# Kernel optimization log

Hardware: AMD Instinct MI355X
Metric: run time of the kernel (lower is better)

## Reference

```python
import jax, jax.numpy as jnp
import numpy as np

B, L, D, H, E, M, P = 2, 512, 768, 12, 32, 4, 256
EMB, BS, MAP, C = 768, 64, 256, 97


def setup_inputs() -> dict:
    key = jax.random.key(0)
    ks = jax.random.split(key, 16)
    w = lambda k, s: (0.02 * jax.random.normal(k, s, jnp.float32))
    seq = jax.random.normal(ks[0], (B, L, D), jnp.float32)
    attn = jax.random.uniform(ks[1], (B, H, L, L), jnp.float32)
    entity_pos = jax.random.randint(ks[2], (B, E, M), 0, L - 2)
    # distinct (h, t) entity pairs per document -> unique mention-pair scatter slots
    grid = jnp.stack(jnp.meshgrid(jnp.arange(E), jnp.arange(E), indexing='ij'), -1).reshape(-1, 2)
    hts = jnp.stack([grid[jax.random.permutation(jax.random.fold_in(ks[3], b), E * E)[:P]] for b in range(B)], 0)
    mention_idx = jnp.broadcast_to(jnp.arange(E * M).reshape(E, M), (B, E, M))
    return {
        'seq': seq, 'attn': attn,
        'entity_pos': entity_pos, 'hts': hts, 'mention_idx': mention_idx,
        'W_head': w(ks[4], (2 * D, EMB)), 'b_head': jnp.zeros((EMB,), jnp.float32),
        'W_tail': w(ks[5], (2 * D, EMB)), 'b_tail': jnp.zeros((EMB,), jnp.float32),
        'W_rel': w(ks[6], (EMB * BS, C)), 'b_rel': jnp.zeros((C,), jnp.float32),
        'W_fh': w(ks[7], (D, EMB)), 'W_ft': w(ks[8], (D, EMB)), 'b_f': jnp.zeros((EMB,), jnp.float32),
        'W_unet': w(ks[9], (EMB, C)), 'b_unet': jnp.zeros((C,), jnp.float32),
        'W_mlp': w(ks[10], (EMB, C)), 'b_mlp': jnp.zeros((C,), jnp.float32),
        'W_bil': w(ks[11], (3 * C, C)), 'b_bil': jnp.zeros((C,), jnp.float32),
    }


def reference(seq, attn, entity_pos, hts, mention_idx,
              W_head, b_head, W_tail, b_tail, W_rel, b_rel,
              W_fh, W_ft, b_f, W_unet, b_unet, W_mlp, b_mlp, W_bil, b_bil):
    pos = entity_pos + 1                                 # bert offset
    b3 = jnp.arange(B)[:, None, None]
    ment_emb = seq[b3, pos]                              # [B,E,M,D] mention gather
    ment_att = attn[b3, :, pos]                          # [B,E,M,H,L]
    ent_emb = jax.nn.logsumexp(ment_emb, axis=2)         # [B,E,D] logsumexp pool
    ent_att = ment_att.mean(axis=2)                      # [B,E,H,L]
    b2 = jnp.arange(B)[:, None]
    h_idx, t_idx = hts[..., 0], hts[..., 1]
    hs, ts = ent_emb[b2, h_idx], ent_emb[b2, t_idx]      # [B,P,D]
    ha, ta = ent_att[b2, h_idx], ent_att[b2, t_idx]      # [B,P,H,L]
    ht_att = (ha * ta).mean(2)                           # [B,P,L]
    ht_att = ht_att / (ht_att.sum(-1, keepdims=True) + 1e-5)
    rs = jnp.einsum('bld,bpl->bpd', seq, ht_att)         # localized context
    N = B * P
    hz = jnp.tanh(jnp.concatenate([hs, rs], -1).reshape(N, 2 * D) @ W_head + b_head)
    tz = jnp.tanh(jnp.concatenate([ts, rs], -1).reshape(N, 2 * D) @ W_tail + b_tail)
    bl = (hz.reshape(N, EMB // BS, BS, 1) * tz.reshape(N, EMB // BS, 1, BS)).reshape(N, EMB * BS)
    r1 = bl @ W_rel + b_rel                              # [N,C]
    # mention-pair dense map scatter (map_rss)
    ment_flat = ment_emb.reshape(B, E * M, D)
    mh = mention_idx[b2, h_idx]                          # [B,P,M]
    mt = mention_idx[b2, t_idx]
    mh2 = jnp.broadcast_to(mh[:, :, :, None], (B, P, M, M))
    mt2 = jnp.broadcast_to(mt[:, :, None, :], (B, P, M, M))
    b4 = jnp.broadcast_to(jnp.arange(B)[:, None, None, None], (B, P, M, M))
    eh = ment_flat[b4, mh2]                              # [B,P,M,M,D]
    et = ment_flat[b4, mt2]
    feat = eh @ W_fh + et @ W_ft + b_f                   # fused Linear(cat(h,t))
    mp = jnp.zeros((B, MAP, MAP, EMB), seq.dtype).at[b4, mh2, mt2].set(feat)
    enc2 = jnp.tanh(mp @ W_unet + b_unet)                # UNet-channel surrogate
    enc3 = jax.nn.gelu(mp @ W_mlp + b_mlp)               # MLP-channel surrogate
    r2 = jax.nn.logsumexp(enc2[b4, mh2, mt2], axis=(2, 3)).reshape(N, C)
    r3 = jax.nn.logsumexp(enc3[b4, mh2, mt2], axis=(2, 3)).reshape(N, C)
    return jnp.concatenate([r1, r2, r3], -1) @ W_bil + b_bil
```

## Files before the change

kernel.cpp:

```cpp
#include <hip/hip_runtime.h>
#include <hip/hip_bf16.h>

#define B_  2
#define L_  512
#define D_  768
#define H_  12
#define E_  32
#define M_  4
#define P_  256
#define EMB_ 768
#define BS_ 64
#define C_  97
#define N_  (B_*P_)

#define KTOT_    49152
#define CPAD_    112
#define KSPLIT_  48
#define KCHUNK_  (KTOT_/KSPLIT_)
#define PSTR_    128
#define TILE_    (CPAD_*64)

typedef __hip_bfloat16 bf16;
typedef __attribute__((ext_vector_type(8))) short bf16x8;
typedef __attribute__((ext_vector_type(4))) float f32x4;
typedef __attribute__((ext_vector_type(8))) float f32x8;

__device__ inline float ldIn(const void* p, long idx, int isbf) {
    return isbf ? (float)((const bf16*)p)[idx] : ((const float*)p)[idx];
}

__device__ inline unsigned short f2bf(float f) {
    bf16 h = (bf16)f;
    return *(unsigned short*)&h;
}

__device__ inline void cvt16(unsigned short* o, float4 a, float4 b, float4 c, float4 d) {
    o[0]=f2bf(a.x);  o[1]=f2bf(a.y);  o[2]=f2bf(a.z);  o[3]=f2bf(a.w);
    o[4]=f2bf(b.x);  o[5]=f2bf(b.y);  o[6]=f2bf(b.z);  o[7]=f2bf(b.w);
    o[8]=f2bf(c.x);  o[9]=f2bf(c.y);  o[10]=f2bf(c.z); o[11]=f2bf(c.w);
    o[12]=f2bf(d.x); o[13]=f2bf(d.y); o[14]=f2bf(d.z); o[15]=f2bf(d.w);
}

__device__ inline int detect_bf(const void* seqd) {
    const unsigned short* u = (const unsigned short*)seqd;
    int lane = threadIdx.x & 63;
    unsigned short e = (u[lane] >> 7) & 0xFF;
    unsigned long long m = __ballot(e >= 140);
    return m == 0ull;
}

struct PrepArgs {
    const void* src[8];
    long off[8];
    int K[8];
    int Ncols[8];
    int Npad[8];
    unsigned short* dst[8];
    const void* W_bil;  float* W_bilF;
    const void* b_f; const void* W_unet; const void* b_unet;
    const void* W_mlp; const void* b_mlp; float* c23p;
    const void* W_rel; unsigned short* WBt;
    const void* seqd;
    const void* attn; const int* entity_pos; const int* hts;
    unsigned short* mentb; float* ent_emb; unsigned short* htb;
};

union PrepSm {
    float T[32][65];
    unsigned short TW[CPAD_][80];
    float red[256];
};

__global__ void prep_kernel(PrepArgs a) {
    int isbf = detect_bf(a.seqd);
    int z = blockIdx.z;
    __shared__ PrepSm sm;
    int tid = threadIdx.x;
    if (z == 0) {
        int lin = blockIdx.y*48 + blockIdx.x;
        if (lin >= 16) return;
        int c = tid;
        if (c >= C_) return;
        float s2 = 0.f, s3 = 0.f;
        int d0 = lin*48;
        for (int i = 0; i < 48; i++) {
            int d = d0 + i;
            float bf = ldIn(a.b_f, d, isbf);
            s2 += bf * ldIn(a.W_unet, (long)d*C_ + c, isbf);
            s3 += bf * ldIn(a.W_mlp,  (long)d*C_ + c, isbf);
        }
        if (lin == 0) {
            s2 += ldIn(a.b_unet, c, isbf);
            s3 += ldIn(a.b_mlp,  c, isbf);
        }
        a.c23p[lin*194 + c]      = s2;
        a.c23p[lin*194 + 97 + c] = s3;
    } else if (z == 1) {
        int lin = blockIdx.y*48 + blockIdx.x;
        if (lin >= KTOT_/64) return;
        int k0 = lin * 64;
        for (int idx = tid; idx < 64*97; idx += 256) {
            int kk = idx / 97, c = idx % 97;
            sm.TW[c][kk] = f2bf(ldIn(a.W_rel, (long)(k0+kk)*C_ + c, isbf));
        }
        for (int idx = tid; idx < 15*64; idx += 256) {
            sm.TW[97 + (idx>>6)][idx & 63] = 0;
        }
        __syncthreads();
        unsigned short* tb = a.WBt + (long)lin*TILE_;
        for (int t = 0; t < 4; t++) {
            int idx = tid + t*256;
            if (idx < 896) {
                int l  = idx & 63;
                int h  = (idx >> 6) & 1;
                int ct = idx >> 7;
                int row = ct*16 + (l & 15);
                int col = h*32 + (l >> 4)*8;
                *(uint4*)(tb + idx*8) = *(uint4*)&sm.TW[row][col];
            }
        }
    } else if (z <= 9) {
        int j = z - 2;
        int K = a.K[j], Ncols = a.Ncols[j], Npad = a.Npad[j];
        int k0 = blockIdx.x*32, n0 = blockIdx.y*64;
        if (k0 >= K || n0 >= Npad) return;
        const void* src = a.src[j];
        long off = a.off[j];
        unsigned short* dst = a.dst[j];
        int r = tid >> 3, c8 = (tid & 7) * 8;
        if ((Ncols & 7) == 0) {
            long base = off + (long)(k0+r)*Ncols + n0 + c8;
            if (isbf) {
                unsigned short tmp[8];
                *(uint4*)tmp = *(const uint4*)((const unsigned short*)src + base);
                #pragma unroll
                for (int e = 0; e < 8; e++) {
                    bf16 hh = *(bf16*)&tmp[e];
                    sm.T[r][c8+e] = (float)hh;
                }
            } else {
                const float* sp = (const float*)src + base;
                float4 x = *(const float4*)sp;
                float4 y = *(const float4*)(sp + 4);
                sm.T[r][c8+0]=x.x; sm.T[r][c8+1]=x.y; sm.T[r][c8+2]=x.z; sm.T[r][c8+3]=x.w;
                sm.T[r][c8+4]=y.x; sm.T[r][c8+5]=y.y; sm.T[r][c8+6]=y.z; sm.T[r][c8+7]=y.w;
            }
        } else {
            #pragma unroll
            for (int e = 0; e < 8; e++) {
                int n = n0 + c8 + e;
                sm.T[r][c8+e] = (n < Ncols) ? ldIn(src, off + (long)(k0+r)*Ncols + n, isbf) : 0.f;
            }
        }
        __syncthreads();
        int nn = tid >> 2, q8 = (tid & 3) * 8;
        unsigned short o[8];
        #pragma unroll
        for (int e = 0; e < 8; e++) o[e] = f2bf(sm.T[q8+e][nn]);
        *(uint4*)(dst + (long)(n0+nn)*K + k0 + q8) = *(uint4*)o;
    } else if (z == 10) {
        int lin = blockIdx.y*48 + blockIdx.x;
        int idx = lin*256 + tid;
        if (idx < 291*C_) a.W_bilF[idx] = ldIn(a.W_bil, idx, isbf);
    } else {
        int lin = blockIdx.y*48 + blockIdx.x;
        if (lin >= 576) return;
        if (lin < 512) {
            int bp = lin;
            int b = bp >> 8;
            int h_e = a.hts[bp*2+0], t_e = a.hts[bp*2+1];
            int ph[M_], pt[M_];
            for (int m = 0; m < M_; m++) {
                ph[m] = a.entity_pos[(b*E_ + h_e)*M_ + m] + 1;
                pt[m] = a.entity_pos[(b*E_ + t_e)*M_ + m] + 1;
            }
            float v[2];
            for (int t = 0; t < 2; t++) {
                int l = tid + t*256;
                float s = 0.f;
                for (int h = 0; h < H_; h++) {
                    long hb = ((long)(b*H_ + h))*L_;
                    float ha = 0.f, ta = 0.f;
                    for (int m = 0; m < M_; m++) {
                        ha += ldIn(a.attn, (hb + ph[m])*L_ + l, isbf);
                        ta += ldIn(a.attn, (hb + pt[m])*L_ + l, isbf);
                    }
                    s += ha * ta;
                }
                v[t] = s * (0.0625f / H_);
            }
            sm.red[tid] = v[0] + v[1];
            __syncthreads();
            for (int off = 128; off > 0; off >>= 1) {
                if (tid < off) sm.red[tid] += sm.red[tid+off];
                __syncthreads();
            }
            float inv = 1.0f / (sm.red[0] + 1e-5f);
            for (int t = 0; t < 2; t++) {
                int l = tid + t*256;
                a.htb[(long)bp*L_ + l] = f2bf(v[t] * inv);
            }
        } else {
            int be = lin - 512;
            int b = be >> 5;
            int pos[M_];
            for (int m = 0; m < M_; m++) pos[m] = a.entity_pos[be*M_+m] + 1;
            for (int d = tid; d < D_; d += 256) {
                float x[M_];
                for (int m = 0; m < M_; m++) {
                    x[m] = ldIn(a.seqd, ((long)b*L_ + pos[m])*D_ + d, isbf);
                    a.mentb[((long)be*M_ + m)*D_ + d] = f2bf(x[m]);
                }
                float mx = fmaxf(fmaxf(x[0],x[1]), fmaxf(x[2],x[3]));
                float s = expf(x[0]-mx)+expf(x[1]-mx)+expf(x[2]-mx)+expf(x[3]-mx);
                a.ent_emb[(long)be*D_ + d] = mx + logf(s);
            }
        }
    }
}

struct MfmaJob {
    const unsigned short* A[8];
    const unsigned short* Bt[8];
    const void* bias[8];
    void* C[8];
    const void* seqd;
    const int* hts;
    const float* ent_emb;
    const float* rsrc;
    int K[8];
    int ldc[8];
    int act[8];
    int obf[8];
    int Mt[8];
    int Nt[8];
    int gath[8];
};

__global__ void mfma_nt2_kernel(MfmaJob args) {
    int z = blockIdx.z;
    int m0 = blockIdx.x*32, n0 = blockIdx.y*32;
    if (m0 >= args.Mt[z] || n0 >= args.Nt[z]) return;
    int isbf = detect_bf(args.seqd);
    const unsigned short* A  = args.A[z];
    const unsigned short* Bt = args.Bt[z];
    const void* bias = args.bias[z];
    void* C = args.C[z];
    int K = args.K[z], ldc = args.ldc[z], act = args.act[z], obf = args.obf[z];
    int gmode = args.gath[z];
    __shared__ unsigned short Al[2][32][136];
    __shared__ unsigned short Btl[2][32][136];
    int tid = threadIdx.x, wave = tid>>6, lane = tid&63;
    int lm = lane&15, lq = lane>>4;
    int rowg = wave>>1, cgrp = wave&1;
    int rr = tid >> 3;
    int kc = (tid & 7) * 16;
    const float *gh = nullptr, *gr = nullptr;
    if (gmode) {
        int m = m0 + rr, b = m >> 8;
        int ent = args.hts[m*2 + (gmode-1)];
        gh = args.ent_emb + (long)(b*E_ + ent)*D_ + kc;
        gr = args.rsrc + (long)m*EMB_ + kc;
    }
    uint4 ra0, ra1, rb0, rb1;
    float4 fa0, fa1, fa2, fa3;

    if (gmode) {
        fa0 = *(const float4*)gh;      fa1 = *(const float4*)(gh+4);
        fa2 = *(const float4*)(gh+8);  fa3 = *(const float4*)(gh+12);
        unsigned short o[16];
        cvt16(o, fa0, fa1, fa2, fa3);
        *(uint4*)&Al[0][rr][kc]   = *(uint4*)o;
        *(uint4*)&Al[0][rr][kc+8] = *(uint4*)(o+8);
    } else {
        ra0 = *(const uint4*)(A + (long)(m0+rr)*K + kc);
        ra1 = *(const uint4*)(A + (long)(m0+rr)*K + kc + 8);
        *(uint4*)&Al[0][rr][kc]   = ra0;
        *(uint4*)&Al[0][rr][kc+8] = ra1;
    }
    rb0 = *(const uint4*)(Bt + (long)(n0+rr)*K + kc);
    rb1 = *(const uint4*)(Bt + (long)(n0+rr)*K + kc + 8);
    *(uint4*)&Btl[0][rr][kc]   = rb0;
    *(uint4*)&Btl[0][rr][kc+8] = rb1;

    int nst = K >> 7;
    f32x4 acc = {};
    for (int ks = 0; ks < nst; ks++) {
        __syncthreads();
        if (ks+1 < nst) {
            int kk = (ks+1) << 7;
            if (gmode) {
                const float* s = (kk < D_) ? (gh + kk) : (gr + kk - D_);
                fa0 = *(const float4*)s;      fa1 = *(const float4*)(s+4);
                fa2 = *(const float4*)(s+8);  fa3 = *(const float4*)(s+12);
            } else {
                ra0 = *(const uint4*)(A + (long)(m0+rr)*K + kk + kc);
                ra1 = *(const uint4*)(A + (long)(m0+rr)*K + kk + kc + 8);
            }
            rb0 = *(const uint4*)(Bt + (long)(n0+rr)*K + kk + kc);
            rb1 = *(const uint4*)(Bt + (long)(n0+rr)*K + kk + kc + 8);
        }
        int cb = ks & 1;
        #pragma unroll
        for (int half = 0; half < 4; half++) {
            bf16x8 af  = *(bf16x8*)&Al[cb][rowg*16+lm][half*32+lq*8];
            bf16x8 bfr = *(bf16x8*)&Btl[cb][cgrp*16+lm][half*32+lq*8];
            acc = __builtin_amdgcn_mfma_f32_16x16x32_bf16(af, bfr, acc, 0, 0, 0);
        }
        if (ks+1 < nst) {
            int nb = (ks+1) & 1;
            if (gmode) {
                unsigned short o[16];
                cvt16(o, fa0, fa1, fa2, fa3);
                *(uint4*)&Al[nb][rr][kc]   = *(uint4*)o;
                *(uint4*)&Al[nb][rr][kc+8] = *(uint4*)(o+8);
            } else {
                *(uint4*)&Al[nb][rr][kc]   = ra0;
                *(uint4*)&Al[nb][rr][kc+8] = ra1;
            }
            *(uint4*)&Btl[nb][rr][kc]   = rb0;
            *(uint4*)&Btl[nb][rr][kc+8] = rb1;
        }
    }
    int n = n0 + cgrp*16 + lm;
    float bia = bias ? ldIn(bias, n, isbf) : 0.f;
    #pragma unroll
    for (int r = 0; r < 4; r++) {
        int m = m0 + rowg*16 + lq*4 + r;
        float v = acc[r] + bia;
        if (act == 1) v = tanhf(v);
        if (obf) ((unsigned short*)C)[(long)m*ldc + n] = f2bf(v);
        else     ((float*)C)[(long)m*ldc + n] = v;
    }
}

__global__ __launch_bounds__(256, 3)
void r1_mfma_kernel(const float* __restrict__ hz, const float* __restrict__ tz,
                    const unsigned short* __restrict__ WBt,
                    float* __restrict__ partial) {
    __shared__ float hzL[32][17];
    int kz = blockIdx.x;
    int nb0 = blockIdx.y * 32;
    int gk0 = kz * 16;
    int gi0 = kz * 16;
    int g0 = (kz * KCHUNK_) >> 12;
    int tid = threadIdx.x;
    int wave = tid >> 6, lane = tid & 63;
    int lm = lane & 15;
    int ctb = wave * 2;
    int nct = (wave < 3) ? 2 : 1;

    {
        int r = tid >> 3, q = (tid & 7) * 2;
        float2 v = *(const float2*)(hz + (long)(nb0 + r)*EMB_ + gi0 + q);
        hzL[r][q] = v.x; hzL[r][q+1] = v.y;
    }
    int lq = lane >> 4;
    f32x8 tza[2], tzb[2];
    #pragma unroll
    for (int rg = 0; rg < 2; rg++) {
        const float* tp = tz + (long)(nb0 + rg*16 + lm)*EMB_ + g0*64;
        float4 x0 = *(const float4*)(tp + lq*8);
        float4 y0 = *(const float4*)(tp + lq*8 + 4);
        float4 x1 = *(const float4*)(tp + 32 + lq*8);
        float4 y1 = *(const float4*)(tp + 32 + lq*8 + 4);
        tza[rg][0]=x0.x; tza[rg][1]=x0.y; tza[rg][2]=x0.z; tza[rg][3]=x0.w;
        tza[rg][4]=y0.x; tza[rg][5]=y0.y; tza[rg][6]=y0.z; tza[rg][7]=y0.w;
        tzb[rg][0]=x1.x; tzb[rg][1]=x1.y; tzb[rg][2]=x1.z; tzb[rg][3]=x1.w;
        tzb[rg][4]=y1.x; tzb[rg][5]=y1.y; tzb[rg][6]=y1.z; tzb[rg][7]=y1.w;
    }
    __syncthreads();

    const unsigned short* wb = WBt + (long)gk0*TILE_ + lane*8;

    f32x4 acc[2][2] = {};
    bf16x8 cb[2][2];
    #pragma unroll
    for (int ct = 0; ct < 2; ct++)
        if (ct < nct)
            #pragma unroll
            for (int h = 0; h < 2; h++)
                cb[ct][h] = *(const bf16x8*)(wb + ((ctb+ct)*2 + h)*512);

    #pragma unroll 2
    for (int ks = 0; ks < KCHUNK_/64; ks++) {
        bf16x8 nbuf[2][2];
        if (ks+1 < KCHUNK_/64) {
            const unsigned short* wn = wb + (long)(ks+1)*TILE_;
            #pragma unroll
            for (int ct = 0; ct < 2; ct++)
                if (ct < nct)
                    #pragma unroll
                    for (int h = 0; h < 2; h++)
                        nbuf[ct][h] = *(const bf16x8*)(wn + ((ctb+ct)*2 + h)*512);
        }
        float hv0 = hzL[lm][ks];
        float hv1 = hzL[16 + lm][ks];
        unsigned short o00[8], o01[8], o10[8], o11[8];
        #pragma unroll
        for (int e = 0; e < 8; e++) {
            o00[e] = f2bf(tza[0][e] * hv0);
            o01[e] = f2bf(tzb[0][e] * hv0);
            o10[e] = f2bf(tza[1][e] * hv1);
            o11[e] = f2bf(tzb[1][e] * hv1);
        }
        bf16x8 a00 = *(bf16x8*)o00, a01 = *(bf16x8*)o01;
        bf16x8 a10 = *(bf16x8*)o10, a11 = *(bf16x8*)o11;
        #pragma unroll
        for (int ct = 0; ct < 2; ct++) {
            if (ct < nct) {
                acc[ct][0] = __builtin_amdgcn_mfma_f32_16x16x32_bf16(a00, cb[ct][0], acc[ct][0], 0, 0, 0);
                acc[ct][0] = __builtin_amdgcn_mfma_f32_16x16x32_bf16(a01, cb[ct][1], acc[ct][0], 0, 0, 0);
                acc[ct][1] = __builtin_amdgcn_mfma_f32_16x16x32_bf16(a10, cb[ct][0], acc[ct][1], 0, 0, 0);
                acc[ct][1] = __builtin_amdgcn_mfma_f32_16x16x32_bf16(a11, cb[ct][1], acc[ct][1], 0, 0, 0);
            }
        }
        if (ks+1 < KCHUNK_/64) {
            #pragma unroll
            for (int ct = 0; ct < 2; ct++)
                if (ct < nct)
                    #pragma unroll
                    for (int h = 0; h < 2; h++)
                        cb[ct][h] = nbuf[ct][h];
        }
    }
    #pragma unroll
    for (int ct = 0; ct < 2; ct++) {
        if (ct < nct || wave == 3) {
            int c = (ctb + ct)*16 + lm;
            #pragma unroll
            for (int rg = 0; rg < 2; rg++) {
                #pragma unroll
                for (int r = 0; r < 4; r++) {
                    int nl = rg*16 + lq*4 + r;
                    float v = (ct < nct) ? acc[ct][rg][r] : 0.f;
                    partial[((long)(nb0+nl)*KSPLIT_ + kz)*PSTR_ + c] = v;
                }
            }
        }
    }
}

__global__ void r23out_kernel(const float* __restrict__ partial, const void* __restrict__ b_rel,
                              const float* __restrict__ mu, const float* __restrict__ c23p,
                              const int* __restrict__ hts, const int* __restrict__ mention_idx,
                              const float* __restrict__ W_bilF, const void* __restrict__ b_bil,
                              void* __restrict__ out, const void* __restrict__ seqd) {
    int bp = blockIdx.x;
    int b = bp >> 8;
    int c = threadIdx.x;
    int isbf = detect_bf(seqd);
    __shared__ float row[292];
    if (c < C_) {
        const float* pr = partial + (long)bp*KSPLIT_*PSTR_;
        float r1v = 0.f;
        #pragma unroll 8
        for (int kz = 0; kz < KSPLIT_; kz++)
            r1v += pr[kz*PSTR_ + c];
        r1v += ldIn(b_rel, c, isbf);
        int h_e = hts[bp*2+0], t_e = hts[bp*2+1];
        const float* mu2h = mu;
        const float* mu2t = mu + 32768;
        const float* mu3h = mu + 65536;
        const float* mu3t = mu + 98304;
        float ah2[4], at2[4], ah3[4], at3[4];
        for (int m = 0; m < 4; m++) {
            int emh = mention_idx[(b*E_ + h_e)*M_ + m];
            int emt = mention_idx[(b*E_ + t_e)*M_ + m];
            ah2[m] = mu2h[(long)(b*128 + emh)*128 + c];
            ah3[m] = mu3h[(long)(b*128 + emh)*128 + c];
            at2[m] = mu2t[(long)(b*128 + emt)*128 + c];
            at3[m] = mu3t[(long)(b*128 + emt)*128 + c];
        }
        float c2 = 0.f, c3 = 0.f;
        #pragma unroll
        for (int j = 0; j < 16; j++) {
            c2 += c23p[j*194 + c];
            c3 += c23p[j*194 + 97 + c];
        }
        float v2[16], v3[16];
        int q = 0;
        for (int i = 0; i < 4; i++) {
            for (int j = 0; j < 4; j++, q++) {
                float x2 = ah2[i] + at2[j] + c2;
                v2[q] = tanhf(x2);
                float x3 = ah3[i] + at3[j] + c3;
                float t = tanhf(0.7978845608028654f * (x3 + 0.044715f*x3*x3*x3));
                v3[q] = 0.5f * x3 * (1.0f + t);
            }
        }
        float m2 = v2[0], m3 = v3[0];
        for (q = 1; q < 16; q++) { m2 = fmaxf(m2, v2[q]); m3 = fmaxf(m3, v3[q]); }
        float s2 = 0.f, s3 = 0.f;
        for (q = 0; q < 16; q++) { s2 += expf(v2[q]-m2); s3 += expf(v3[q]-m3); }
        row[c]        = r1v;
        row[C_ + c]   = m2 + logf(s2);
        row[2*C_ + c] = m3 + logf(s3);
    }
    __syncthreads();
    if (c >= C_) return;
    float a0 = 0.f, a1 = 0.f, a2 = 0.f, a3 = 0.f;
    #pragma unroll 4
    for (int k = 0; k < 288; k += 4) {
        a0 += row[k+0] * W_bilF[(k+0)*C_ + c];
        a1 += row[k+1] * W_bilF[(k+1)*C_ + c];
        a2 += row[k+2] * W_bilF[(k+2)*C_ + c];
        a3 += row[k+3] * W_bilF[(k+3)*C_ + c];
    }
    a0 += row[288] * W_bilF[288*C_ + c];
    a1 += row[289] * W_bilF[289*C_ + c];
    a2 += row[290] * W_bilF[290*C_ + c];
    float v = a0 + a1 + a2 + a3 + ldIn(b_bil, c, isbf);
    if (isbf) ((bf16*)out)[(long)bp*C_ + c] = (bf16)v;
    else      ((float*)out)[(long)bp*C_ + c] = v;
}

extern "C" void kernel_launch(void* const* d_in, const int* in_sizes, int n_in,
                              void* d_out, int out_size, void* d_ws, size_t ws_size,
                              hipStream_t stream) {
    const void* seq        = d_in[0];
    const void* attn       = d_in[1];
    const int*  entity_pos = (const int*)d_in[2];
    const int*  hts        = (const int*)d_in[3];
    const int*  mention_idx= (const int*)d_in[4];
    const void* W_head     = d_in[5];
    const void* b_head     = d_in[6];
    const void* W_tail     = d_in[7];
    const void* b_tail     = d_in[8];
    const void* W_rel      = d_in[9];
    const void* b_rel      = d_in[10];
    const void* W_fh       = d_in[11];
    const void* W_ft       = d_in[12];
    const void* b_f        = d_in[13];
    const void* W_unet     = d_in[14];
    const void* b_unet     = d_in[15];
    const void* W_mlp      = d_in[16];
    const void* b_mlp      = d_in[17];
    const void* W_bil      = d_in[18];
    const void* b_bil      = d_in[19];

    float* w = (float*)d_ws;
    unsigned short* mentb = (unsigned short*)(w + 64);
    float* ent_emb  = w + 98368;
    unsigned short* htb = (unsigned short*)(w + 540736);
    float* rs       = w + 671808;
    float* hz       = w + 1065024;
    float* tz       = w + 1458240;
    float* mu       = w + 1851456;
    unsigned short* seqT  = (unsigned short*)(w + 1982784);
    unsigned short* WhT   = (unsigned short*)(w + 2376000);
    unsigned short* WtT   = (unsigned short*)(w + 2965824);
    unsigned short* WfhT  = (unsigned short*)(w + 3555648);
    unsigned short* WftT  = (unsigned short*)(w + 3850560);
    unsigned short* WunetT= (unsigned short*)(w + 4145472);
    unsigned short* WmlpT = (unsigned short*)(w + 4194624);
    unsigned short* Tbh   = (unsigned short*)(w + 4243776);
    unsigned short* Tbt   = (unsigned short*)(w + 4342080);
    unsigned short* WBt   = (unsigned short*)(w + 5226816);
    float* partial  = w + 7979328;
    float* c23p     = w + 11200000;
    float* W_bilF   = w + 11649344;

    {
        PrepArgs a = {};
        const void* srcs[8] = {W_head, W_tail, W_fh, W_ft, W_unet, W_mlp, seq, seq};
        long offs[8]   = {0,0,0,0,0,0,0,393216};
        int Ks[8]      = {1536,1536,768,768,768,768,512,512};
        int Ncols8[8]  = {768,768,768,768,97,97,768,768};
        int Npads[8]   = {768,768,768,768,128,128,768,768};
        unsigned short* dsts[8] = {WhT, WtT, WfhT, WftT, WunetT, WmlpT, seqT, seqT+393216};
        for (int z = 0; z < 8; z++) {
            a.src[z]=srcs[z]; a.off[z]=offs[z]; a.K[z]=Ks[z];
            a.Ncols[z]=Ncols8[z]; a.Npad[z]=Npads[z]; a.dst[z]=dsts[z];
        }
        a.W_bil = W_bil; a.W_bilF = W_bilF;
        a.b_f = b_f; a.W_unet = W_unet; a.b_unet = b_unet;
        a.W_mlp = W_mlp; a.b_mlp = b_mlp; a.c23p = c23p;
        a.W_rel = W_rel; a.WBt = WBt;
        a.seqd = seq;
        a.attn = attn; a.entity_pos = entity_pos; a.hts = hts;
        a.mentb = mentb; a.ent_emb = ent_emb; a.htb = htb;
        prep_kernel<<<dim3(48, 16, 12), 256, 0, stream>>>(a);
    }
    {
        MfmaJob ga = {};
        ga.seqd = seq; ga.hts = hts; ga.ent_emb = ent_emb; ga.rsrc = rs;
        for (int z = 0; z < 2; z++) {
            ga.A[z] = htb + (long)z*256*512; ga.Bt[z] = seqT + (long)z*393216;
            ga.bias[z] = nullptr; ga.C[z] = rs + (long)z*256*768;
            ga.K[z] = 512; ga.ldc[z] = 768; ga.act[z] = 0; ga.obf[z] = 0;
            ga.Mt[z] = 256; ga.Nt[z] = 768; ga.gath[z] = 0;
        }
        ga.A[2] = mentb; ga.Bt[2] = WfhT; ga.bias[2] = nullptr; ga.C[2] = Tbh;
        ga.K[2] = 768; ga.ldc[2] = 768; ga.act[2] = 0; ga.obf[2] = 1;
        ga.Mt[2] = 256; ga.Nt[2] = 768; ga.gath[2] = 0;
        ga.A[3] = mentb; ga.Bt[3] = WftT; ga.bias[3] = nullptr; ga.C[3] = Tbt;
        ga.K[3] = 768; ga.ldc[3] = 768; ga.act[3] = 0; ga.obf[3] = 1;
        ga.Mt[3] = 256; ga.Nt[3] = 768; ga.gath[3] = 0;
        mfma_nt2_kernel<<<dim3(8, 24, 4), 256, 0, stream>>>(ga);
    }
    {
        MfmaJob ga = {};
        ga.seqd = seq; ga.hts = hts; ga.ent_emb = ent_emb; ga.rsrc = rs;
        ga.A[0] = nullptr; ga.Bt[0] = WhT; ga.bias[0] = b_head; ga.C[0] = hz;
        ga.A[1] = nullptr; ga.Bt[1] = WtT; ga.bias[1] = b_tail; ga.C[1] = tz;
        for (int z = 0; z < 2; z++) {
            ga.K[z] = 1536; ga.ldc[z] = 768; ga.act[z] = 1; ga.obf[z] = 0;
            ga.Mt[z] = 512; ga.Nt[z] = 768; ga.gath[z] = z + 1;
        }
        const unsigned short* As[4] = {Tbh, Tbt, Tbh, Tbt};
        const unsigned short* Bs[4] = {WunetT, WunetT, WmlpT, WmlpT};
        for (int q = 0; q < 4; q++) {
            int z = 2 + q;
            ga.A[z] = As[q]; ga.Bt[z] = Bs[q]; ga.bias[z] = nullptr;
            ga.C[z] = mu + q*32768;
            ga.K[z] = 768; ga.ldc[z] = 128; ga.act[z] = 0; ga.obf[z] = 0;
            ga.Mt[z] = 256; ga.Nt[z] = 128; ga.gath[z] = 0;
        }
        mfma_nt2_kernel<<<dim3(16, 24, 6), 256, 0, stream>>>(ga);
    }
    r1_mfma_kernel<<<dim3(KSPLIT_, 16), 256, 0, stream>>>(hz, tz, WBt, partial);
    r23out_kernel<<<N_, 128, 0, stream>>>(partial, b_rel, mu, c23p, hts, mention_idx,
                                          W_bilF, b_bil, d_out, seq);
}
```

Before: 208.1 us.

## Precompute per-entity attention means before pair products to avoid redundant attn reads

The old pair-attention path recomputed mention sums of the full attention rows for every head/tail pair, reading 8 rows per head per pair from the large attn tensor. It now computes per-entity mean attention once in prep (768 entity-head blocks), and a new small kernel forms the pair products and normalisation from that cache. The mention-embedding gather and logsumexp work moves into spare z==0 blocks. This removes heavily redundant global reads at the cost of an extra kernel launch and an intermediate fp32 buffer.

```diff
diff --git a/kernel.cpp b/kernel.cpp
--- a/kernel.cpp
+++ b/kernel.cpp
@@ -61,14 +61,13 @@
     const void* W_mlp; const void* b_mlp; float* c23p;
     const void* W_rel; unsigned short* WBt;
     const void* seqd;
-    const void* attn; const int* entity_pos; const int* hts;
-    unsigned short* mentb; float* ent_emb; unsigned short* htb;
+    const void* attn; const int* entity_pos;
+    unsigned short* mentb; float* ent_emb; float* ent_att;
 };
 
 union PrepSm {
     float T[32][65];
     unsigned short TW[CPAD_][80];
-    float red[256];
 };
 
 __global__ void prep_kernel(PrepArgs a) {
@@ -78,23 +77,39 @@
     int tid = threadIdx.x;
     if (z == 0) {
         int lin = blockIdx.y*48 + blockIdx.x;
-        if (lin >= 16) return;
-        int c = tid;
-        if (c >= C_) return;
-        float s2 = 0.f, s3 = 0.f;
-        int d0 = lin*48;
-        for (int i = 0; i < 48; i++) {
-            int d = d0 + i;
-            float bf = ldIn(a.b_f, d, isbf);
-            s2 += bf * ldIn(a.W_unet, (long)d*C_ + c, isbf);
-            s3 += bf * ldIn(a.W_mlp,  (long)d*C_ + c, isbf);
-        }
-        if (lin == 0) {
-            s2 += ldIn(a.b_unet, c, isbf);
-            s3 += ldIn(a.b_mlp,  c, isbf);
-        }
-        a.c23p[lin*194 + c]      = s2;
-        a.c23p[lin*194 + 97 + c] = s3;
+        if (lin < 16) {
+            int c = tid;
+            if (c >= C_) return;
+            float s2 = 0.f, s3 = 0.f;
+            int d0 = lin*48;
+            for (int i = 0; i < 48; i++) {
+                int d = d0 + i;
+                float bf = ldIn(a.b_f, d, isbf);
+                s2 += bf * ldIn(a.W_unet, (long)d*C_ + c, isbf);
+                s3 += bf * ldIn(a.W_mlp,  (long)d*C_ + c, isbf);
+            }
+            if (lin == 0) {
+                s2 += ldIn(a.b_unet, c, isbf);
+                s3 += ldIn(a.b_mlp,  c, isbf);
+            }
+            a.c23p[lin*194 + c]      = s2;
+            a.c23p[lin*194 + 97 + c] = s3;
+        } else if (lin >= 64 && lin < 128) {
+            int be = lin - 64;
+            int b = be >> 5;
+            int pos[M_];
+            for (int m = 0; m < M_; m++) pos[m] = a.entity_pos[be*M_+m] + 1;
+            for (int d = tid; d < D_; d += 256) {
+                float x[M_];
+                for (int m = 0; m < M_; m++) {
+                    x[m] = ldIn(a.seqd, ((long)b*L_ + pos[m])*D_ + d, isbf);
+                    a.mentb[((long)be*M_ + m)*D_ + d] = f2bf(x[m]);
+                }
+                float mx = fmaxf(fmaxf(x[0],x[1]), fmaxf(x[2],x[3]));
+                float s = expf(x[0]-mx)+expf(x[1]-mx)+expf(x[2]-mx)+expf(x[3]-mx);
+                a.ent_emb[(long)be*D_ + d] = mx + logf(s);
+            }
+        }
     } else if (z == 1) {
         int lin = blockIdx.y*48 + blockIdx.x;
         if (lin >= KTOT_/64) return;
@@ -163,59 +178,48 @@
         int idx = lin*256 + tid;
         if (idx < 291*C_) a.W_bilF[idx] = ldIn(a.W_bil, idx, isbf);
     } else {
-        int lin = blockIdx.y*48 + blockIdx.x;
-        if (lin >= 576) return;
-        if (lin < 512) {
-            int bp = lin;
-            int b = bp >> 8;
-            int h_e = a.hts[bp*2+0], t_e = a.hts[bp*2+1];
-            int ph[M_], pt[M_];
-            for (int m = 0; m < M_; m++) {
-                ph[m] = a.entity_pos[(b*E_ + h_e)*M_ + m] + 1;
-                pt[m] = a.entity_pos[(b*E_ + t_e)*M_ + m] + 1;
-            }
-            float v[2];
-            for (int t = 0; t < 2; t++) {
-                int l = tid + t*256;
-                float s = 0.f;
-                for (int h = 0; h < H_; h++) {
-                    long hb = ((long)(b*H_ + h))*L_;
-                    float ha = 0.f, ta = 0.f;
-                    for (int m = 0; m < M_; m++) {
-                        ha += ldIn(a.attn, (hb + ph[m])*L_ + l, isbf);
-                        ta += ldIn(a.attn, (hb + pt[m])*L_ + l, isbf);
-                    }
-                    s += ha * ta;
-                }
-                v[t] = s * (0.0625f / H_);
-            }
-            sm.red[tid] = v[0] + v[1];
-            __syncthreads();
-            for (int off = 128; off > 0; off >>= 1) {
-                if (tid < off) sm.red[tid] += sm.red[tid+off];
-                __syncthreads();
-            }
-            float inv = 1.0f / (sm.red[0] + 1e-5f);
-            for (int t = 0; t < 2; t++) {
-                int l = tid + t*256;
-                a.htb[(long)bp*L_ + l] = f2bf(v[t] * inv);
-            }
-        } else {
-            int be = lin - 512;
-            int b = be >> 5;
-            int pos[M_];
-            for (int m = 0; m < M_; m++) pos[m] = a.entity_pos[be*M_+m] + 1;
-            for (int d = tid; d < D_; d += 256) {
-                float x[M_];
-                for (int m = 0; m < M_; m++) {
-                    x[m] = ldIn(a.seqd, ((long)b*L_ + pos[m])*D_ + d, isbf);
-                    a.mentb[((long)be*M_ + m)*D_ + d] = f2bf(x[m]);
-                }
-                float mx = fmaxf(fmaxf(x[0],x[1]), fmaxf(x[2],x[3]));
-                float s = expf(x[0]-mx)+expf(x[1]-mx)+expf(x[2]-mx)+expf(x[3]-mx);
-                a.ent_emb[(long)be*D_ + d] = mx + logf(s);
-            }
-        }
+        int beh = blockIdx.y*48 + blockIdx.x;
+        if (beh >= 768) return;
+        int h = beh % H_;
+        int be = beh / H_;
+        int b = be >> 5;
+        int pos[M_];
+        for (int m = 0; m < M_; m++) pos[m] = a.entity_pos[be*M_+m] + 1;
+        for (int t = 0; t < 2; t++) {
+            int l = tid + t*256;
+            float s = 0.f;
+            for (int m = 0; m < M_; m++)
+                s += ldIn(a.attn, (((long)(b*H_ + h))*L_ + pos[m])*L_ + l, isbf);
+            a.ent_att[(long)beh*L_ + l] = 0.25f * s;
+        }
+    }
+}
+
+__global__ void htatt_kernel(const float* __restrict__ ent_att, const int* __restrict__ hts,
+                             unsigned short* __restrict__ htb) {
+    int bp = blockIdx.x;
+    int b = bp >> 8;
+    int h_e = hts[bp*2+0], t_e = hts[bp*2+1];
+    const float* ea_h = ent_att + (long)((b*E_ + h_e)*H_)*L_;
+    const float* ea_t = ent_att + (long)((b*E_ + t_e)*H_)*L_;
+    __shared__ float red[256];
+    float v[2];
+    for (int t = 0; t < 2; t++) {
+        int l = threadIdx.x + t*256;
+        float s = 0.f;
+        for (int h = 0; h < H_; h++) s += ea_h[h*L_+l] * ea_t[h*L_+l];
+        v[t] = s * (1.0f/H_);
+    }
+    red[threadIdx.x] = v[0] + v[1];
+    __syncthreads();
+    for (int off = 128; off > 0; off >>= 1) {
+        if (threadIdx.x < off) red[threadIdx.x] += red[threadIdx.x+off];
+        __syncthreads();
+    }
+    float inv = 1.0f / (red[0] + 1e-5f);
+    for (int t = 0; t < 2; t++) {
+        int l = threadIdx.x + t*256;
+        htb[(long)bp*L_ + l] = f2bf(v[t] * inv);
     }
 }
 
@@ -542,6 +546,7 @@
     float* w = (float*)d_ws;
     unsigned short* mentb = (unsigned short*)(w + 64);
     float* ent_emb  = w + 98368;
+    float* ent_att  = w + 147520;
     unsigned short* htb = (unsigned short*)(w + 540736);
     float* rs       = w + 671808;
     float* hz       = w + 1065024;
@@ -578,10 +583,11 @@
         a.W_mlp = W_mlp; a.b_mlp = b_mlp; a.c23p = c23p;
         a.W_rel = W_rel; a.WBt = WBt;
         a.seqd = seq;
-        a.attn = attn; a.entity_pos = entity_pos; a.hts = hts;
-        a.mentb = mentb; a.ent_emb = ent_emb; a.htb = htb;
+        a.attn = attn; a.entity_pos = entity_pos;
+        a.mentb = mentb; a.ent_emb = ent_emb; a.ent_att = ent_att;
         prep_kernel<<<dim3(48, 16, 12), 256, 0, stream>>>(a);
     }
+    htatt_kernel<<<N_, 256, 0, stream>>>(ent_att, hts, htb);
     {
         MfmaJob ga = {};
         ga.seqd = seq; ga.hts = hts; ga.ent_emb = ent_emb; ga.rsrc = rs;
```

Result: faster. 200.2 us (-3.8%).
